# Performance work log

Hardware: AMD Instinct MI355X
Metric: run time of the kernel (lower is better)

## Reference

```python
import jax, jax.numpy as jnp
import numpy as np

N = 65536      # nodes
E = 1048576    # edges (avg degree 16)
L = 24         # input_length == lstm input size == lstm num_layers
H = 64         # lstm hidden


def _lin_init(key, fi, fo):
    return jax.random.normal(key, (fi, fo), jnp.float32) / np.sqrt(fi)


def setup_inputs() -> dict:
    key = jax.random.key(0)
    ks = iter(jax.random.split(key, 64))
    d = {}
    d["x"] = jax.random.normal(next(ks), (N, 421 + L), jnp.float32)
    d["edge_index"] = jax.random.randint(next(ks), (2, E), 0, N)

    def lin(fi, fo):
        return _lin_init(next(ks), fi, fo), jnp.zeros((fo,), jnp.float32)

    d["poi1_W"], d["poi1_b"] = lin(13, 64)
    d["poi2_W"], d["poi2_b"] = lin(64, 64)
    d["svi1_W"], d["svi1_b"] = lin(365, 128)
    d["svi2_W"], d["svi2_b"] = lin(128, 128)
    d["all1_W"], d["all1_b"] = lin(192, 128)
    d["all2_W"], d["all2_b"] = lin(128, 128)
    for name, fi, fo in (("gat1", 128, 128), ("gat2", 128, 128), ("gat3", 128, 64)):
        d[name + "_W"], d[name + "_b"] = lin(fi, fo)
        d[name + "_asrc"] = jax.random.normal(next(ks), (fo,), jnp.float32) / np.sqrt(fo)
        d[name + "_adst"] = jax.random.normal(next(ks), (fo,), jnp.float32) / np.sqrt(fo)
    d["lstm_Wih0"] = jax.random.normal(next(ks), (L, 4 * H), jnp.float32) / np.sqrt(L)
    d["lstm_Wih"] = jax.random.normal(next(ks), (L - 1, H, 4 * H), jnp.float32) / np.sqrt(H)
    d["lstm_Whh"] = jax.random.normal(next(ks), (L, H, 4 * H), jnp.float32) / np.sqrt(H)
    d["lstm_b"] = jnp.zeros((L, 4 * H), jnp.float32)
    d["time1_W"], d["time1_b"] = lin(64, 64)
    d["time2_W"], d["time2_b"] = lin(64, 64)
    d["lin1_W"], d["lin1_b"] = lin(128, 64)
    d["lin2_W"], d["lin2_b"] = lin(64, 64)
    d["lin3_W"], d["lin3_b"] = lin(64, 1)
    return d


def _gat(h_in, W, a_src, a_dst, b, src, dst, n):
    # PyG GATConv (1 head): gather -> per-edge attn -> segment softmax -> scatter
    h = h_in @ W                                   # [N, F]
    s = h @ a_src                                  # [N]
    t = h @ a_dst                                  # [N]
    e = jax.nn.leaky_relu(s[src] + t[dst], 0.2)    # [E']
    m = jax.ops.segment_max(e, dst, num_segments=n)
    ee = jnp.exp(e - m[dst])
    denom = jax.ops.segment_sum(ee, dst, num_segments=n)
    alpha = ee / denom[dst]
    out = jax.ops.segment_sum(h[src] * alpha[:, None], dst, num_segments=n)
    return out + b


def _forward(x, poi1_W, poi1_b, poi2_W, poi2_b, svi1_W, svi1_b, svi2_W, svi2_b,
             all1_W, all1_b, all2_W, all2_b,
             gat1_W, gat1_b, gat1_asrc, gat1_adst,
             gat2_W, gat2_b, gat2_asrc, gat2_adst,
             gat3_W, gat3_b, gat3_asrc, gat3_adst,
             lstm_Wih0, lstm_Wih, lstm_Whh, lstm_b,
             time1_W, time1_b, time2_W, time2_b,
             lin1_W, lin1_b, lin2_W, lin2_b, lin3_W, lin3_b,
             edge_index):
    n = x.shape[0]
    relu = jax.nn.relu
    # feature-branch MLPs
    x_poi = relu(relu(x[:, 3:16] @ poi1_W + poi1_b) @ poi2_W + poi2_b)
    x_svi = relu(relu(x[:, 56:421] @ svi1_W + svi1_b) @ svi2_W + svi2_b)
    h = jnp.concatenate([x_poi, x_svi], axis=1)
    h = relu(relu(h @ all1_W + all1_b) @ all2_W + all2_b)
    # add self loops once (PyG GATConv default add_self_loops=True)
    loops = jnp.arange(n, dtype=edge_index.dtype)
    src = jnp.concatenate([edge_index[0], loops])
    dst = jnp.concatenate([edge_index[1], loops])
    h = relu(_gat(h, gat1_W, gat1_asrc, gat1_adst, gat1_b, src, dst, n))
    h = relu(_gat(h, gat2_W, gat2_asrc, gat2_adst, gat2_b, src, dst, n))
    h = relu(_gat(h, gat3_W, gat3_asrc, gat3_adst, gat3_b, src, dst, n))
    # stacked LSTM over the single timestep t (h0=c0=0 -> f gate & Whh contribute 0)
    inp = x[:, 421:]                               # [N, L]
    hs = []
    for l in range(L):
        Wih = lstm_Wih0 if l == 0 else lstm_Wih[l - 1]
        gates = inp @ Wih + lstm_b[l]              # [N, 4H], torch gate order i,f,g,o
        i, f, g, o = jnp.split(gates, 4, axis=-1)
        c = jax.nn.sigmoid(i) * jnp.tanh(g)
        h_l = jax.nn.sigmoid(o) * jnp.tanh(c)
        hs.append(h_l)
        inp = h_l
    t = hs[2]                                      # hn[2]
    t = relu(relu(t @ time1_W + time1_b) @ time2_W + time2_b)
    z = jnp.concatenate([h, t], axis=1)            # [N, 128]
    z = relu(z @ lin1_W + lin1_b)
    z = relu(z @ lin2_W + lin2_b)
    return z @ lin3_W + lin3_b                     # [N, 1]


def reference(x, edge_index, poi1_W, poi1_b, poi2_W, poi2_b, svi1_W, svi1_b,
              svi2_W, svi2_b, all1_W, all1_b, all2_W, all2_b,
              gat1_W, gat1_b, gat1_asrc, gat1_adst,
              gat2_W, gat2_b, gat2_asrc, gat2_adst,
              gat3_W, gat3_b, gat3_asrc, gat3_adst,
              lstm_Wih0, lstm_Wih, lstm_Whh, lstm_b,
              time1_W, time1_b, time2_W, time2_b,
              lin1_W, lin1_b, lin2_W, lin2_b, lin3_W, lin3_b):
    return _forward(x, poi1_W, poi1_b, poi2_W, poi2_b, svi1_W, svi1_b, svi2_W, svi2_b,
                    all1_W, all1_b, all2_W, all2_b,
                    gat1_W, gat1_b, gat1_asrc, gat1_adst,
                    gat2_W, gat2_b, gat2_asrc, gat2_adst,
                    gat3_W, gat3_b, gat3_asrc, gat3_adst,
                    lstm_Wih0, lstm_Wih, lstm_Whh, lstm_b,
                    time1_W, time1_b, time2_W, time2_b,
                    lin1_W, lin1_b, lin2_W, lin2_b, lin3_W, lin3_b,
                    edge_index)
```

## Files before the change

### kernel.cpp

```cpp
#include <hip/hip_runtime.h>
#include <math.h>

#define DEV __device__ __forceinline__

typedef __attribute__((ext_vector_type(8))) short short8;
typedef __attribute__((ext_vector_type(4))) float f32x4;
typedef float f32x4u __attribute__((ext_vector_type(4), aligned(4)));
typedef __attribute__((ext_vector_type(4))) unsigned int u32x4;
typedef __attribute__((ext_vector_type(4))) _Float16 h16x4;

#define NEG_BIG (-3.0e38f)
#define CAPB 4096
#define CHUNK 4096

DEV float sigm(float x) { return 1.0f / (1.0f + __expf(-x)); }
DEV float leaky(float e) { return (e >= 0.0f) ? e : 0.2f * e; }

DEV void split_bf16(const float f[8], short8& hi, short8& lo) {
#pragma unroll
  for (int i = 0; i < 8; ++i) {
    unsigned u = __builtin_bit_cast(unsigned, f[i]);
    hi[i] = (short)(u >> 16);
    float h = __builtin_bit_cast(float, u & 0xffff0000u);
    float r = f[i] - h;
    lo[i] = (short)(__builtin_bit_cast(unsigned, r) >> 16);
  }
}

DEV unsigned packsplit(float v) {
  unsigned u = __builtin_bit_cast(unsigned, v);
  unsigned hf = u & 0xffff0000u;
  float r = v - __builtin_bit_cast(float, hf);
  return hf | (__builtin_bit_cast(unsigned, r) >> 16);
}

DEV void unpack_pk(const u32x4 p0, const u32x4 p1, short8& hi, short8& lo) {
  u32x4 h, l;
  h[0] = __builtin_amdgcn_perm(p0[1], p0[0], 0x07060302u);
  h[1] = __builtin_amdgcn_perm(p0[3], p0[2], 0x07060302u);
  h[2] = __builtin_amdgcn_perm(p1[1], p1[0], 0x07060302u);
  h[3] = __builtin_amdgcn_perm(p1[3], p1[2], 0x07060302u);
  l[0] = __builtin_amdgcn_perm(p0[1], p0[0], 0x05040100u);
  l[1] = __builtin_amdgcn_perm(p0[3], p0[2], 0x05040100u);
  l[2] = __builtin_amdgcn_perm(p1[1], p1[0], 0x05040100u);
  l[3] = __builtin_amdgcn_perm(p1[3], p1[2], 0x05040100u);
  hi = __builtin_bit_cast(short8, h);
  lo = __builtin_bit_cast(short8, l);
}

template <int G, int MT, int NT>
DEV void mfma_grp(f32x4 (&acc)[MT][NT], const short8 (&ah)[MT],
                  const short8 (&al)[MT], const short8 (&bh)[4],
                  const short8 (&bl)[4]) {
#pragma unroll
  for (int mt = 0; mt < MT; ++mt)
#pragma unroll
    for (int j = 0; j < 4; ++j) {
      acc[mt][G * 4 + j] = __builtin_amdgcn_mfma_f32_16x16x32_bf16(
          ah[mt], bh[j], acc[mt][G * 4 + j], 0, 0, 0);
      acc[mt][G * 4 + j] = __builtin_amdgcn_mfma_f32_16x16x32_bf16(
          ah[mt], bl[j], acc[mt][G * 4 + j], 0, 0, 0);
      acc[mt][G * 4 + j] = __builtin_amdgcn_mfma_f32_16x16x32_bf16(
          al[mt], bh[j], acc[mt][G * 4 + j], 0, 0, 0);
    }
}


__global__ void fill_i32_kernel(int* p, int v, int n) {
  int i = blockIdx.x * blockDim.x + threadIdx.x;
  if (i < n) p[i] = v;
}


__global__ __launch_bounds__(256) void bucket_bin(
    const int* __restrict__ ei, int* __restrict__ bucket_cnt,
    unsigned* __restrict__ ebuf, int E, int Et) {
  __shared__ unsigned stage[CHUNK];
  __shared__ int hist[512], rbase[512], lcur[512];
  const int tid = threadIdx.x;
  const long long e0 = (long long)blockIdx.x * CHUNK;
  const int nalive = (int)((Et - e0) < CHUNK ? (Et - e0) : CHUNK);
  for (int i = tid; i < 512; i += 256) hist[i] = 0;
  __syncthreads();
  for (int k = tid; k < nalive; k += 256) {
    long long e = e0 + k;
    int s, d;
    if (e < E) { s = ei[e]; d = ei[E + e]; } else { s = (int)(e - E); d = s; }
    unsigned p = (unsigned)s | ((unsigned)d << 16);
    stage[k] = p;
    atomicAdd(&hist[d >> 7], 1);
  }
  __syncthreads();
  for (int i = tid; i < 512; i += 256) {
    int c = hist[i];
    rbase[i] = c ? atomicAdd(&bucket_cnt[i], c) : 0;
    lcur[i] = 0;
  }
  __syncthreads();
  for (int k = tid; k < nalive; k += 256) {
    unsigned p = stage[k];
    int b = (int)(p >> 23);
    int lofs = atomicAdd(&lcur[b], 1);
    int pos = rbase[b] + lofs;
    if (pos < CAPB) ebuf[(long long)b * CAPB + pos] = p;
  }
}

__global__ __launch_bounds__(512) void bucket_scan(
    const int* __restrict__ cnt, int* __restrict__ start, int Et) {
  __shared__ int sh[512];
  int tid = threadIdx.x;
  int v = cnt[tid];
  sh[tid] = v;
  __syncthreads();
  int val = v;
  for (int off = 1; off < 512; off <<= 1) {
    int add = (tid >= off) ? sh[tid - off] : 0;
    __syncthreads();
    val += add;
    sh[tid] = val;
    __syncthreads();
  }
  start[tid] = val - v;
  if (tid == 511) start[512] = Et;
}

__global__ __launch_bounds__(128) void bucket_csr(
    const unsigned* __restrict__ ebuf, const int* __restrict__ bucket_cnt,
    const int* __restrict__ bucket_start, int* __restrict__ row_start,
    int* __restrict__ srcs, int N, int Et) {
  __shared__ unsigned stage[CAPB];
  __shared__ int hist[128], hbase[128], lcur[128];
  const int b = blockIdx.x, tid = threadIdx.x;
  int cnt = bucket_cnt[b];
  cnt = cnt < CAPB ? cnt : CAPB;
  const int gbase = bucket_start[b];
  hist[tid] = 0;
  __syncthreads();
  const unsigned* eb = ebuf + (long long)b * CAPB;
  for (int k = tid; k < cnt; k += 128) {
    unsigned p = eb[k];
    stage[k] = p;
    atomicAdd(&hist[(p >> 16) & 127], 1);
  }
  __syncthreads();
  int v = hist[tid];
  hbase[tid] = v;
  __syncthreads();
  int val = v;
  for (int off = 1; off < 128; off <<= 1) {
    int add = (tid >= off) ? hbase[tid - off] : 0;
    __syncthreads();
    val += add;
    hbase[tid] = val;
    __syncthreads();
  }
  int ex = val - v;
  row_start[b * 128 + tid] = gbase + ex;
  __syncthreads();
  hbase[tid] = ex;
  lcur[tid] = 0;
  __syncthreads();
  for (int k = tid; k < cnt; k += 128) {
    unsigned p = stage[k];
    int o = (p >> 16) & 127;
    int lofs = atomicAdd(&lcur[o], 1);
    srcs[gbase + hbase[o] + lofs] = (int)(p & 0xffffu);
  }
  if (b == 0 && tid == 0) row_start[N] = Et;
}

struct WJobs {
  const float* W[16];
  short* hi[16];
  short* lo[16];
  int K[16];
  int M16[16];
  int ldw[16];
  int skip[16];
  int tile0[16];
};

__global__ __launch_bounds__(64) void wsplit_all(WJobs jb, int njobs) {
  int b = blockIdx.x;
  int ji = 0;
#pragma unroll
  for (int i = 1; i < 16; ++i)
    if (i < njobs && b >= jb.tile0[i]) ji = i;
  int t = b - jb.tile0[ji];
  int M16 = jb.M16[ji];
  int kc = t / M16, ntG = t % M16;
  int K = jb.K[ji], ldw = jb.ldw[ji];
  const float* __restrict__ W = jb.W[ji];

  int lane = threadIdx.x;
  int kb = kc * 32 + (lane >> 4) * 8;
  int c = ntG * 16 + (lane & 15);
  if (jb.skip[ji] && c >= 64) c += 64;
  float f[8];
#pragma unroll
  for (int j = 0; j < 8; ++j) {
    int k = kb + j;
    f[j] = (k < K) ? W[(long long)k * ldw + c] : 0.0f;
  }
  short8 h, l;
  split_bf16(f, h, l);
  long long off = ((long long)t * 64 + lane) * 8;
  *(short8*)(jb.hi[ji] + off) = h;
  *(short8*)(jb.lo[ji] + off) = l;
}


template <int MT, int NT, int APK>
DEV void gemm_loop(const void* __restrict__ Av, long long abase, int lda,
                   const short* __restrict__ wh, const short* __restrict__ wl,
                   int K, int KC, f32x4 (&acc)[MT][NT]) {
  const int lane = threadIdx.x;
  const int m = lane & 15, q = lane >> 4;
#pragma unroll
  for (int i = 0; i < MT; ++i)
#pragma unroll
    for (int j = 0; j < NT; ++j) acc[i][j] = (f32x4)(0.0f);

  u32x4 pA[MT][2];
  float fA[MT][8];

  auto loadA = [&](int kc) {
#pragma unroll
    for (int mt = 0; mt < MT; ++mt) {
      if (APK == 1) {
        const unsigned* ap =
            (const unsigned*)Av + (abase + mt * 16 + m) * lda + kc * 32 + q * 8;
        pA[mt][0] = *(const u32x4*)ap;
        pA[mt][1] = *(const u32x4*)(ap + 4);
      } else {
        const float* ap =
            (const float*)Av + (abase + mt * 16 + m) * lda + kc * 32 + q * 8;
        if (kc * 32 + 32 <= K) {
          f32x4u p0 = *(const f32x4u*)ap;
          f32x4u p1 = *(const f32x4u*)(ap + 4);
#pragma unroll
          for (int j = 0; j < 4; ++j) { fA[mt][j] = p0[j]; fA[mt][4 + j] = p1[j]; }
        } else {
#pragma unroll
          for (int j = 0; j < 8; ++j) {
            int k = kc * 32 + q * 8 + j;
            fA[mt][j] = (k < K) ? ap[j] : 0.0f;
          }
        }
      }
    }
  };

  short8 ah[MT], al[MT];
  auto unpackA = [&]() {
#pragma unroll
    for (int mt = 0; mt < MT; ++mt) {
      if (APK == 1)
        unpack_pk(pA[mt][0], pA[mt][1], ah[mt], al[mt]);
      else
        split_bf16(fA[mt], ah[mt], al[mt]);
    }
  };

  short8 bh0[4], bl0[4], bh1[4], bl1[4];
  auto loadB = [&](short8 (&bh)[4], short8 (&bl)[4], int kc, int gg) {
#pragma unroll
    for (int j = 0; j < 4; ++j) {
      long long off = (((long long)kc * NT + (gg * 4 + j)) * 64 + lane) * 8;
      bh[j] = *(const short8*)(wh + off);
      bl[j] = *(const short8*)(wl + off);
    }
  };

  if constexpr (NT == 4) {
    loadA(0);
    loadB(bh0, bl0, 0, 0);
    int kc = 0;
    for (; kc + 2 <= KC; kc += 2) {
      unpackA();
      loadB(bh1, bl1, kc + 1, 0);
      loadA(kc + 1);
      mfma_grp<0, MT, NT>(acc, ah, al, bh0, bl0);
      unpackA();
      if (kc + 2 < KC) {
        loadB(bh0, bl0, kc + 2, 0);
        loadA(kc + 2);
      }
      mfma_grp<0, MT, NT>(acc, ah, al, bh1, bl1);
    }
    if (kc < KC) {
      unpackA();
      mfma_grp<0, MT, NT>(acc, ah, al, bh0, bl0);
    }
  } else {
    loadA(0);
    loadB(bh0, bl0, 0, 0);
    for (int kc = 0; kc < KC; ++kc) {
      unpackA();
      loadB(bh1, bl1, kc, 1);
      if (kc + 1 < KC) loadA(kc + 1);
      mfma_grp<0, MT, NT>(acc, ah, al, bh0, bl0);
      if (kc + 1 < KC) loadB(bh0, bl0, kc + 1, 0);
      mfma_grp<1, MT, NT>(acc, ah, al, bh1, bl1);
    }
  }
}


template <int MT, int NT>
DEV void epi_packed(const f32x4 (&acc)[MT][NT], const float* bias,
                    unsigned* C, int ldc, long long r0, int act) {
  const int lane = threadIdx.x;
  const int m = lane & 15, q = lane >> 4;
#pragma unroll
  for (int nt = 0; nt < NT; ++nt) {
    int col = nt * 16 + m;
    float b = bias ? bias[col] : 0.0f;
#pragma unroll
    for (int mt = 0; mt < MT; ++mt) {
      long long rb = r0 + mt * 16 + q * 4;
#pragma unroll
      for (int reg = 0; reg < 4; ++reg) {
        float v = acc[mt][nt][reg] + b;
        if (act) v = fmaxf(v, 0.0f);
        C[(rb + reg) * ldc + col] = packsplit(v);
      }
    }
  }
}

template <int MT, int NT>
DEV void epi_lds(const f32x4 (&acc)[MT][NT], const float* bias,
                 unsigned* L, int S) {
  const int lane = threadIdx.x;
  const int m = lane & 15, q = lane >> 4;
#pragma unroll
  for (int nt = 0; nt < NT; ++nt) {
    int col = nt * 16 + m;
    float b = bias[col];
#pragma unroll
    for (int mt = 0; mt < MT; ++mt)
#pragma unroll
      for (int reg = 0; reg < 4; ++reg) {
        float v = fmaxf(acc[mt][nt][reg] + b, 0.0f);
        L[(mt * 16 + q * 4 + reg) * S + col] = packsplit(v);
      }
  }
}

struct GemmArgs {
  const void* A; const short* wh; const short* wl; const float* bias;
  void* C; const float* asrc; const float* adst; float* sOut; float* tOut;
  int lda, ldc, K, KC, act;
};

template <int MT, int NT, int APK, int OPK, int STE>
__global__ __launch_bounds__(64) void gemm_mfma(GemmArgs g) {
  const int lane = threadIdx.x;
  const int m = lane & 15, q = lane >> 4;
  const long long r0 = (long long)blockIdx.x * (MT * 16);
  f32x4 acc[MT][NT];
  gemm_loop<MT, NT, APK>(g.A, r0, g.lda, g.wh, g.wl, g.K, g.KC, acc);

#pragma unroll
  for (int nt = 0; nt < NT; ++nt) {
    int col = nt * 16 + m;
    float bsv = g.bias ? g.bias[col] : 0.0f;
#pragma unroll
    for (int mt = 0; mt < MT; ++mt) {
      long long rb = r0 + mt * 16 + q * 4;
#pragma unroll
      for (int reg = 0; reg < 4; ++reg) {
        float v = acc[mt][nt][reg] + bsv;
        if (g.act == 1) v = fmaxf(v, 0.0f);
        if (OPK == 1)
          ((unsigned*)g.C)[(rb + reg) * g.ldc + col] = packsplit(v);
        else if (OPK == 2)
          ((_Float16*)g.C)[(rb + reg) * g.ldc + col] = (_Float16)v;
        else
          ((float*)g.C)[(rb + reg) * g.ldc + col] = v;
      }
    }
  }

  if (STE == 1) {
    float as[NT], ad[NT];
#pragma unroll
    for (int nt = 0; nt < NT; ++nt) {
      int col = nt * 16 + m;
      as[nt] = g.asrc[col];
      ad[nt] = g.adst[col];
    }
#pragma unroll
    for (int mt = 0; mt < MT; ++mt)
#pragma unroll
      for (int reg = 0; reg < 4; ++reg) {
        float ps = 0.0f, pt = 0.0f;
#pragma unroll
        for (int nt = 0; nt < NT; ++nt) {
          ps = fmaf(acc[mt][nt][reg], as[nt], ps);
          pt = fmaf(acc[mt][nt][reg], ad[nt], pt);
        }
#pragma unroll
        for (int off = 1; off < 16; off <<= 1) {
          ps += __shfl_xor(ps, off, 64);
          pt += __shfl_xor(pt, off, 64);
        }
        if (m == 0) {
          long long r = r0 + mt * 16 + q * 4 + reg;
          g.sOut[r] = ps;
          g.tOut[r] = pt;
        }
      }
  }
}


struct PairJob {
  const void* A; int lda, K1;
  const short *w1h, *w1l; const float* b1;
  const short *w2h, *w2l; const float* b2; int K2;
  unsigned* C; int ldc;
};

template <int NT1, int APK1, int NT2>
DEV void pair_body(const PairJob& j, int bid, unsigned* lbuf) {
  constexpr int S = NT1 * 16 + 4;
  const long long r0 = (long long)bid * 32;
  {
    f32x4 acc[2][NT1];
    gemm_loop<2, NT1, APK1>(j.A, r0, j.lda, j.w1h, j.w1l, j.K1,
                            (j.K1 + 31) / 32, acc);
    epi_lds<2, NT1>(acc, j.b1, lbuf, S);
  }
  {
    f32x4 acc[2][NT2];
    gemm_loop<2, NT2, 1>(lbuf, 0, S, j.w2h, j.w2l, j.K2, (j.K2 + 31) / 32, acc);
    epi_packed<2, NT2>(acc, j.b2, j.C, j.ldc, r0, 1);
  }
}

template <int NT1, int APK1, int NT2>
__global__ __launch_bounds__(64) void pair_kernel(PairJob j) {
  __shared__ __align__(16) unsigned lbuf[32 * 132];
  pair_body<NT1, APK1, NT2>(j, blockIdx.x, lbuf);
}


struct ChainJob {
  const float* x; int lda;
  const short *w0h, *w0l; const float* b0;
  const short *w1h, *w1l; const float* b1;
  const short *w2h, *w2l; const float* b2;
  const short *t1h, *t1l; const float* tb1;
  const short *t2h, *t2l; const float* tb2;
  unsigned* C; int ldc;
};

template <int APK>
DEV void lstm_loop(const void* __restrict__ Av, long long abase, int lda,
                   const short* __restrict__ wh, const short* __restrict__ wl,
                   int K, int KC, f32x4 (&acc)[12]) {
  const int lane = threadIdx.x;
  const int m = lane & 15, q = lane >> 4;
#pragma unroll
  for (int j = 0; j < 12; ++j) acc[j] = (f32x4)(0.0f);

  u32x4 pA[2];
  float fA[8];

  auto loadA = [&](int kc) {
    if (APK == 1) {
      const unsigned* ap =
          (const unsigned*)Av + (abase + m) * lda + kc * 32 + q * 8;
      pA[0] = *(const u32x4*)ap;
      pA[1] = *(const u32x4*)(ap + 4);
    } else {
      const float* ap = (const float*)Av + (abase + m) * lda + kc * 32 + q * 8;
      if (kc * 32 + 32 <= K) {
        f32x4u p0 = *(const f32x4u*)ap;
        f32x4u p1 = *(const f32x4u*)(ap + 4);
#pragma unroll
        for (int j = 0; j < 4; ++j) { fA[j] = p0[j]; fA[4 + j] = p1[j]; }
      } else {
#pragma unroll
        for (int j = 0; j < 8; ++j) {
          int k = kc * 32 + q * 8 + j;
          fA[j] = (k < K) ? ap[j] : 0.0f;
        }
      }
    }
  };

  short8 bh0, bl0, bh1, bl1;
  auto loadB = [&](short8& bh, short8& bl, int kc, int nt) {
    long long off = (((long long)kc * 12 + nt) * 64 + lane) * 8;
    bh = *(const short8*)(wh + off);
    bl = *(const short8*)(wl + off);
  };

  loadA(0);
  loadB(bh0, bl0, 0, 0);
  for (int kc = 0; kc < KC; ++kc) {
    short8 ah, al;
    if (APK == 1)
      unpack_pk(pA[0], pA[1], ah, al);
    else
      split_bf16(fA, ah, al);
    loadB(bh1, bl1, kc, 1);
    if (kc + 1 < KC) loadA(kc + 1);
    const int kn = (kc + 1 < KC) ? kc + 1 : kc;
#pragma unroll
    for (int nt = 0; nt < 12; ++nt) {
      short8& cbh = (nt & 1) ? bh1 : bh0;
      short8& cbl = (nt & 1) ? bl1 : bl0;
      acc[nt] = __builtin_amdgcn_mfma_f32_16x16x32_bf16(ah, cbh, acc[nt], 0, 0, 0);
      acc[nt] = __builtin_amdgcn_mfma_f32_16x16x32_bf16(ah, cbl, acc[nt], 0, 0, 0);
      acc[nt] = __builtin_amdgcn_mfma_f32_16x16x32_bf16(al, cbh, acc[nt], 0, 0, 0);
      if (nt + 2 < 12)
        loadB((nt & 1) ? bh1 : bh0, (nt & 1) ? bl1 : bl0, kc, nt + 2);
      else if (nt + 2 == 12)
        loadB(bh0, bl0, kn, 0);
    }
  }
}

DEV void lstm_epi_lds(const f32x4 (&acc)[12], const float* bias,
                      unsigned* L, int S) {
  const int lane = threadIdx.x;
  const int m = lane & 15, q = lane >> 4;
#pragma unroll
  for (int nt = 0; nt < 4; ++nt) {
    int col = nt * 16 + m;
    float bi = bias[col], bg = bias[128 + col], bo = bias[192 + col];
#pragma unroll
    for (int reg = 0; reg < 4; ++reg) {
      float gi = acc[nt][reg] + bi;
      float gg = acc[nt + 4][reg] + bg;
      float go = acc[nt + 8][reg] + bo;
      float cc = sigm(gi) * tanhf(gg);
      L[(q * 4 + reg) * S + col] = packsplit(sigm(go) * tanhf(cc));
    }
  }
}

DEV void chain_body(const ChainJob& c, int bid, unsigned* lbuf) {
  constexpr int S = 68;
  const long long r0 = (long long)bid * 16;
  unsigned* H0 = lbuf;
  unsigned* H1 = lbuf + 16 * S;
  {
    f32x4 acc[12];
    lstm_loop<0>(c.x, r0, c.lda, c.w0h, c.w0l, 24, 1, acc);
    lstm_epi_lds(acc, c.b0, H0, S);
  }
  {
    f32x4 acc[12];
    lstm_loop<1>(H0, 0, S, c.w1h, c.w1l, 64, 2, acc);
    lstm_epi_lds(acc, c.b1, H1, S);
  }
  {
    f32x4 acc[12];
    lstm_loop<1>(H1, 0, S, c.w2h, c.w2l, 64, 2, acc);
    lstm_epi_lds(acc, c.b2, H0, S);
  }
  {
    f32x4 acc[1][4];
    gemm_loop<1, 4, 1>(H0, 0, S, c.t1h, c.t1l, 64, 2, acc);
    epi_lds<1, 4>(acc, c.tb1, H1, S);
  }
  {
    f32x4 acc[1][4];
    gemm_loop<1, 4, 1>(H1, 0, S, c.t2h, c.t2l, 64, 2, acc);
    epi_packed<1, 4>(acc, c.tb2, c.C, c.ldc, r0, 1);
  }
}


__global__ __launch_bounds__(64) void tower_combo(PairJob svi, PairJob poi,
                                                  ChainJob ch, int nA, int nAB) {
  __shared__ __align__(16) unsigned lbuf[32 * 132];
  int bid = blockIdx.x;
  if (bid < nA)
    pair_body<8, 0, 8>(svi, bid, lbuf);
  else if (bid < nAB)
    pair_body<4, 0, 4>(poi, bid - nA, lbuf);
  else
    chain_body(ch, bid - nAB, lbuf);
}


struct HeadJob {
  const void* A; int lda, K1;
  const short *w1h, *w1l; const float* b1;
  const short *w2h, *w2l; const float* b2; int K2;
  const float* w3; const float* b3; float* out;
};

__global__ __launch_bounds__(64) void head_kernel(HeadJob j) {
  __shared__ __align__(16) unsigned lbuf[32 * 68];
  constexpr int S = 68;
  const int lane = threadIdx.x;
  const int m = lane & 15, q = lane >> 4;
  const long long r0 = (long long)blockIdx.x * 32;
  {
    f32x4 acc[2][4];
    gemm_loop<2, 4, 1>(j.A, r0, j.lda, j.w1h, j.w1l, j.K1, (j.K1 + 31) / 32, acc);
    epi_lds<2, 4>(acc, j.b1, lbuf, S);
  }
  {
    f32x4 acc[2][4];
    gemm_loop<2, 4, 1>(lbuf, 0, S, j.w2h, j.w2l, j.K2, (j.K2 + 31) / 32, acc);
    float w3[4], bs[4];
#pragma unroll
    for (int nt = 0; nt < 4; ++nt) {
      int col = nt * 16 + m;
      w3[nt] = j.w3[col];
      bs[nt] = j.b2[col];
    }
#pragma unroll
    for (int mt = 0; mt < 2; ++mt)
#pragma unroll
      for (int reg = 0; reg < 4; ++reg) {
        float ps = 0.0f;
#pragma unroll
        for (int nt = 0; nt < 4; ++nt) {
          float v = fmaxf(acc[mt][nt][reg] + bs[nt], 0.0f);
          ps = fmaf(v, w3[nt], ps);
        }
#pragma unroll
        for (int off = 1; off < 16; off <<= 1) ps += __shfl_xor(ps, off, 64);
        if (m == 0) j.out[r0 + mt * 16 + q * 4 + reg] = ps + j.b3[0];
      }
  }
}


template <int FO, int OPK>
__global__ __launch_bounds__(256) void gat_agg(
    const _Float16* __restrict__ G, const float* __restrict__ s,
    const float* __restrict__ t, const int* __restrict__ row_start,
    const int* __restrict__ srcs, const float* __restrict__ bias,
    void* __restrict__ outv, int ldc) {
  constexpr int CAP = 128;
  constexpr int LPE = FO / 4;
  constexpr int EPW = 64 / LPE;
  __shared__ float ecache[4][CAP];
  __shared__ int icache[4][CAP];
  const int wv = threadIdx.x >> 6;
  const int lane = threadIdx.x & 63;
  const int d = blockIdx.x * 4 + wv;
  const int start = row_start[d], end = row_start[d + 1];
  const float td = t[d];

  float m = NEG_BIG, dsum = 0.0f;
  for (int j = start + lane; j < end; j += 64) {
    int sj = srcs[j];
    float e = leaky(s[sj] + td);
    int idx = j - start;
    if (idx < CAP) { ecache[wv][idx] = e; icache[wv][idx] = sj; }
    float mn = fmaxf(m, e);
    dsum = dsum * __expf(m - mn) + __expf(e - mn);
    m = mn;
  }
#pragma unroll
  for (int off = 32; off; off >>= 1) {
    float mo = __shfl_xor(m, off, 64);
    float dso = __shfl_xor(dsum, off, 64);
    float mn = fmaxf(m, mo);
    dsum = dsum * __expf(m - mn) + dso * __expf(mo - mn);
    m = mn;
  }
  const float inv = 1.0f / dsum;

  const int deg = end - start;
  const int capdeg = deg < CAP ? deg : CAP;
  for (int idx = lane; idx < capdeg; idx += 64)
    ecache[wv][idx] = __expf(ecache[wv][idx] - m) * inv;
  __syncthreads();

  const int grp = lane / LPE, cl = lane % LPE;
  const _Float16* __restrict__ Gc = G + cl * 4;
  float a0 = 0.0f, a1 = 0.0f, a2 = 0.0f, a3 = 0.0f;
  int idx = grp;
  for (; idx + 3 * EPW < capdeg; idx += 4 * EPW) {
    const int i1 = idx + EPW, i2 = idx + 2 * EPW, i3 = idx + 3 * EPW;
    int s0 = icache[wv][idx], s1 = icache[wv][i1];
    int s2 = icache[wv][i2], s3 = icache[wv][i3];
    float l0 = ecache[wv][idx], l1 = ecache[wv][i1];
    float l2 = ecache[wv][i2], l3 = ecache[wv][i3];
    h16x4 g0 = *(const h16x4*)(Gc + (long long)s0 * FO);
    h16x4 g1 = *(const h16x4*)(Gc + (long long)s1 * FO);
    h16x4 g2 = *(const h16x4*)(Gc + (long long)s2 * FO);
    h16x4 g3 = *(const h16x4*)(Gc + (long long)s3 * FO);
    a0 = fmaf(l0, (float)g0[0], a0); a1 = fmaf(l0, (float)g0[1], a1);
    a2 = fmaf(l0, (float)g0[2], a2); a3 = fmaf(l0, (float)g0[3], a3);
    a0 = fmaf(l1, (float)g1[0], a0); a1 = fmaf(l1, (float)g1[1], a1);
    a2 = fmaf(l1, (float)g1[2], a2); a3 = fmaf(l1, (float)g1[3], a3);
    a0 = fmaf(l2, (float)g2[0], a0); a1 = fmaf(l2, (float)g2[1], a1);
    a2 = fmaf(l2, (float)g2[2], a2); a3 = fmaf(l2, (float)g2[3], a3);
    a0 = fmaf(l3, (float)g3[0], a0); a1 = fmaf(l3, (float)g3[1], a1);
    a2 = fmaf(l3, (float)g3[2], a2); a3 = fmaf(l3, (float)g3[3], a3);
  }
  for (; idx + EPW < capdeg; idx += 2 * EPW) {
    const int i1 = idx + EPW;
    int s0 = icache[wv][idx], s1 = icache[wv][i1];
    float l0 = ecache[wv][idx], l1 = ecache[wv][i1];
    h16x4 g0 = *(const h16x4*)(Gc + (long long)s0 * FO);
    h16x4 g1 = *(const h16x4*)(Gc + (long long)s1 * FO);
    a0 = fmaf(l0, (float)g0[0], a0); a1 = fmaf(l0, (float)g0[1], a1);
    a2 = fmaf(l0, (float)g0[2], a2); a3 = fmaf(l0, (float)g0[3], a3);
    a0 = fmaf(l1, (float)g1[0], a0); a1 = fmaf(l1, (float)g1[1], a1);
    a2 = fmaf(l1, (float)g1[2], a2); a3 = fmaf(l1, (float)g1[3], a3);
  }
  for (; idx < capdeg; idx += EPW) {
    int s0 = icache[wv][idx];
    float l0 = ecache[wv][idx];
    h16x4 g0 = *(const h16x4*)(Gc + (long long)s0 * FO);
    a0 = fmaf(l0, (float)g0[0], a0); a1 = fmaf(l0, (float)g0[1], a1);
    a2 = fmaf(l0, (float)g0[2], a2); a3 = fmaf(l0, (float)g0[3], a3);
  }
  for (; idx < deg; idx += EPW) {
    int s0 = srcs[start + idx];
    float l0 = __expf(leaky(s[s0] + td) - m) * inv;
    h16x4 g0 = *(const h16x4*)(Gc + (long long)s0 * FO);
    a0 = fmaf(l0, (float)g0[0], a0); a1 = fmaf(l0, (float)g0[1], a1);
    a2 = fmaf(l0, (float)g0[2], a2); a3 = fmaf(l0, (float)g0[3], a3);
  }
#pragma unroll
  for (int off = 32; off >= LPE; off >>= 1) {
    a0 += __shfl_xor(a0, off, 64);
    a1 += __shfl_xor(a1, off, 64);
    a2 += __shfl_xor(a2, off, 64);
    a3 += __shfl_xor(a3, off, 64);
  }
  if (grp == 0) {
    f32x4u bs = *(const f32x4u*)(bias + cl * 4);
    float v0 = fmaxf(a0 + bs[0], 0.0f);
    float v1 = fmaxf(a1 + bs[1], 0.0f);
    float v2 = fmaxf(a2 + bs[2], 0.0f);
    float v3 = fmaxf(a3 + bs[3], 0.0f);
    if (OPK == 1) {
      u32x4 pv;
      pv[0] = packsplit(v0); pv[1] = packsplit(v1);
      pv[2] = packsplit(v2); pv[3] = packsplit(v3);
      *(u32x4*)((unsigned*)outv + (long long)d * ldc + cl * 4) = pv;
    } else {
      f32x4u v; v[0] = v0; v[1] = v1; v[2] = v2; v[3] = v3;
      *(f32x4u*)((float*)outv + (long long)d * ldc + cl * 4) = v;
    }
  }
}


struct WSplit { const short* hi; const short* lo; };

extern "C" void kernel_launch(void* const* d_in, const int* in_sizes, int n_in,
                              void* d_out, int out_size, void* d_ws, size_t ws_size,
                              hipStream_t stream) {
  const int N = 65536, E = 1048576;
  const int Et = E + N;

  const float* x        = (const float*)d_in[0];
  const int*   ei       = (const int*)d_in[1];
  const float* poi1_W   = (const float*)d_in[2];
  const float* poi1_b   = (const float*)d_in[3];
  const float* poi2_W   = (const float*)d_in[4];
  const float* poi2_b   = (const float*)d_in[5];
  const float* svi1_W   = (const float*)d_in[6];
  const float* svi1_b   = (const float*)d_in[7];
  const float* svi2_W   = (const float*)d_in[8];
  const float* svi2_b   = (const float*)d_in[9];
  const float* all1_W   = (const float*)d_in[10];
  const float* all1_b   = (const float*)d_in[11];
  const float* all2_W   = (const float*)d_in[12];
  const float* all2_b   = (const float*)d_in[13];
  const float* gat1_W   = (const float*)d_in[14];
  const float* gat1_b   = (const float*)d_in[15];
  const float* gat1_as  = (const float*)d_in[16];
  const float* gat1_ad  = (const float*)d_in[17];
  const float* gat2_W   = (const float*)d_in[18];
  const float* gat2_b   = (const float*)d_in[19];
  const float* gat2_as  = (const float*)d_in[20];
  const float* gat2_ad  = (const float*)d_in[21];
  const float* gat3_W   = (const float*)d_in[22];
  const float* gat3_b   = (const float*)d_in[23];
  const float* gat3_as  = (const float*)d_in[24];
  const float* gat3_ad  = (const float*)d_in[25];
  const float* lstm_Wih0= (const float*)d_in[26];
  const float* lstm_Wih = (const float*)d_in[27];
  const float* lstm_b   = (const float*)d_in[29];
  const float* time1_W  = (const float*)d_in[30];
  const float* time1_b  = (const float*)d_in[31];
  const float* time2_W  = (const float*)d_in[32];
  const float* time2_b  = (const float*)d_in[33];
  const float* lin1_W   = (const float*)d_in[34];
  const float* lin1_b   = (const float*)d_in[35];
  const float* lin2_W   = (const float*)d_in[36];
  const float* lin2_b   = (const float*)d_in[37];
  const float* lin3_W   = (const float*)d_in[38];
  const float* lin3_b   = (const float*)d_in[39];
  float* out = (float*)d_out;

  float* wsf   = (float*)d_ws;
  float* R192  = wsf;
  float* RA    = R192 + (size_t)N * 192;
  float* RB    = RA + (size_t)N * 128;
  float* Rz    = RB + (size_t)N * 128;
  float* sArr  = Rz + (size_t)N * 128;
  float* tArr  = sArr + N;
  int* ints         = (int*)(tArr + N);
  int* row_start    = ints;
  int* srcs         = row_start + (N + 1);
  int* bucket_cnt   = srcs + Et;
  int* bucket_start = bucket_cnt + 512;
  unsigned* ebuf    = (unsigned*)(bucket_start + 513);
  short* pool = (short*)(((uintptr_t)(ebuf + 512 * CAPB) + 15) & ~(uintptr_t)15);

  WJobs jb{};
  int nj = 0, tiles = 0;
  auto split = [&](const float* W, int K, int M, int ldw, int skip) -> WSplit {
    int KC = (K + 31) / 32;
    size_t sz = (size_t)KC * M * 32;
    short* hi = pool; pool += sz;
    short* lo = pool; pool += sz;
    jb.W[nj] = W; jb.hi[nj] = hi; jb.lo[nj] = lo;
    jb.K[nj] = K; jb.M16[nj] = M / 16; jb.ldw[nj] = ldw; jb.skip[nj] = skip;
    jb.tile0[nj] = tiles;
    tiles += KC * (M / 16);
    ++nj;
    return {hi, lo};
  };

  auto mkg = [&](const void* A, int lda, WSplit w, const float* bias, void* C,
                 int ldc, int K, int act, const float* as_ = nullptr,
                 const float* ad_ = nullptr, float* sO = nullptr,
                 float* tO = nullptr) -> GemmArgs {
    GemmArgs g;
    g.A = A; g.lda = lda; g.wh = w.hi; g.wl = w.lo; g.bias = bias;
    g.C = C; g.ldc = ldc; g.K = K; g.KC = (K + 31) / 32; g.act = act;
    g.asrc = as_; g.adst = ad_; g.sOut = sO; g.tOut = tO;
    return g;
  };

  WSplit wpoi1 = split(poi1_W, 13, 64, 64, 0);
  WSplit wpoi2 = split(poi2_W, 64, 64, 64, 0);
  WSplit wsvi1 = split(svi1_W, 365, 128, 128, 0);
  WSplit wsvi2 = split(svi2_W, 128, 128, 128, 0);
  WSplit wall1 = split(all1_W, 192, 128, 128, 0);
  WSplit wall2 = split(all2_W, 128, 128, 128, 0);
  WSplit wg1   = split(gat1_W, 128, 128, 128, 0);
  WSplit wg2   = split(gat2_W, 128, 128, 128, 0);
  WSplit wg3   = split(gat3_W, 128, 64, 64, 0);
  WSplit wls0  = split(lstm_Wih0, 24, 192, 256, 1);
  WSplit wls1  = split(lstm_Wih, 64, 192, 256, 1);
  WSplit wls2  = split(lstm_Wih + 64 * 256, 64, 192, 256, 1);
  WSplit wt1   = split(time1_W, 64, 64, 64, 0);
  WSplit wt2   = split(time2_W, 64, 64, 64, 0);
  WSplit wl1   = split(lin1_W, 128, 64, 64, 0);
  WSplit wl2   = split(lin2_W, 64, 64, 64, 0);
  hipLaunchKernelGGL(wsplit_all, dim3(tiles), dim3(64), 0, stream, jb, nj);

  const int TB = 256;
  const int GB = N / 32;
  const int CB = N / 16;

  hipLaunchKernelGGL(fill_i32_kernel, dim3(2), dim3(TB), 0, stream,
                     bucket_cnt, 0, 512);
  hipLaunchKernelGGL(bucket_bin, dim3((Et + CHUNK - 1) / CHUNK), dim3(256),
                     0, stream, ei, bucket_cnt, ebuf, E, Et);
  hipLaunchKernelGGL(bucket_scan, dim3(1), dim3(512), 0, stream,
                     bucket_cnt, bucket_start, Et);
  hipLaunchKernelGGL(bucket_csr, dim3(512), dim3(128), 0, stream,
                     ebuf, bucket_cnt, bucket_start, row_start, srcs, N, Et);

  _Float16* Gh = (_Float16*)RA;

  PairJob svi;
  svi.A = x + 56; svi.lda = 445; svi.K1 = 365;
  svi.w1h = wsvi1.hi; svi.w1l = wsvi1.lo; svi.b1 = svi1_b;
  svi.w2h = wsvi2.hi; svi.w2l = wsvi2.lo; svi.b2 = svi2_b; svi.K2 = 128;
  svi.C = (unsigned*)R192 + 64; svi.ldc = 192;
  PairJob poi;
  poi.A = x + 3; poi.lda = 445; poi.K1 = 13;
  poi.w1h = wpoi1.hi; poi.w1l = wpoi1.lo; poi.b1 = poi1_b;
  poi.w2h = wpoi2.hi; poi.w2l = wpoi2.lo; poi.b2 = poi2_b; poi.K2 = 64;
  poi.C = (unsigned*)R192; poi.ldc = 192;
  ChainJob ch;
  ch.x = x + 421; ch.lda = 445;
  ch.w0h = wls0.hi; ch.w0l = wls0.lo; ch.b0 = lstm_b;
  ch.w1h = wls1.hi; ch.w1l = wls1.lo; ch.b1 = lstm_b + 256;
  ch.w2h = wls2.hi; ch.w2l = wls2.lo; ch.b2 = lstm_b + 512;
  ch.t1h = wt1.hi; ch.t1l = wt1.lo; ch.tb1 = time1_b;
  ch.t2h = wt2.hi; ch.t2l = wt2.lo; ch.tb2 = time2_b;
  ch.C = (unsigned*)Rz + 64; ch.ldc = 128;
  hipLaunchKernelGGL(tower_combo, dim3(GB + GB + CB), dim3(64), 0, stream,
                     svi, poi, ch, GB, GB + GB);

  PairJob allp;
  allp.A = R192; allp.lda = 192; allp.K1 = 192;
  allp.w1h = wall1.hi; allp.w1l = wall1.lo; allp.b1 = all1_b;
  allp.w2h = wall2.hi; allp.w2l = wall2.lo; allp.b2 = all2_b; allp.K2 = 128;
  allp.C = (unsigned*)RB; allp.ldc = 128;
  hipLaunchKernelGGL((pair_kernel<8, 1, 8>), dim3(GB), dim3(64), 0, stream,
                     allp);

  const int aggBlocks = N / 4;

  hipLaunchKernelGGL((gemm_mfma<2, 8, 1, 2, 1>), dim3(GB), dim3(64), 0, stream,
                     mkg(RB, 128, wg1, nullptr, Gh, 128, 128, 0,
                         gat1_as, gat1_ad, sArr, tArr));
  hipLaunchKernelGGL((gat_agg<128, 1>), dim3(aggBlocks), dim3(256), 0, stream,
                     Gh, sArr, tArr, row_start, srcs, gat1_b, RB, 128);
  hipLaunchKernelGGL((gemm_mfma<2, 8, 1, 2, 1>), dim3(GB), dim3(64), 0, stream,
                     mkg(RB, 128, wg2, nullptr, Gh, 128, 128, 0,
                         gat2_as, gat2_ad, sArr, tArr));
  hipLaunchKernelGGL((gat_agg<128, 1>), dim3(aggBlocks), dim3(256), 0, stream,
                     Gh, sArr, tArr, row_start, srcs, gat2_b, RB, 128);
  hipLaunchKernelGGL((gemm_mfma<2, 4, 1, 2, 1>), dim3(GB), dim3(64), 0, stream,
                     mkg(RB, 128, wg3, nullptr, Gh, 64, 128, 0,
                         gat3_as, gat3_ad, sArr, tArr));
  hipLaunchKernelGGL((gat_agg<64, 1>), dim3(aggBlocks), dim3(256), 0, stream,
                     Gh, sArr, tArr, row_start, srcs, gat3_b, Rz, 128);

  HeadJob hd;
  hd.A = Rz; hd.lda = 128; hd.K1 = 128;
  hd.w1h = wl1.hi; hd.w1l = wl1.lo; hd.b1 = lin1_b;
  hd.w2h = wl2.hi; hd.w2l = wl2.lo; hd.b2 = lin2_b; hd.K2 = 64;
  hd.w3 = lin3_W; hd.b3 = lin3_b; hd.out = out;
  hipLaunchKernelGGL(head_kernel, dim3(GB), dim3(64), 0, stream, hd);
}
```

Before: 583.0 us.

## Fuse GAT aggregation with next layer's projection GEMM in one kernel

Adds an agg_gemm kernel in which four waves each aggregate four destination rows into an LDS tile. Wave 0 then runs the next GAT layer's MFMA projection on that tile and also computes the attention scalars s and t. This removes the round trip of writing aggregated features to global memory and reading them back in separate gemm launches, and cuts two launches. In exchange, three of the four waves sit idle during the GEMM phase, and ping-pong buffers (Gh2, sB, tB) are added so the fused kernel never overwrites the inputs it is still reading.

```diff
diff --git a/kernel.cpp b/kernel.cpp
--- a/kernel.cpp
+++ b/kernel.cpp
@@ -215,7 +215,7 @@
 DEV void gemm_loop(const void* __restrict__ Av, long long abase, int lda,
                    const short* __restrict__ wh, const short* __restrict__ wl,
                    int K, int KC, f32x4 (&acc)[MT][NT]) {
-  const int lane = threadIdx.x;
+  const int lane = threadIdx.x & 63;
   const int m = lane & 15, q = lane >> 4;
 #pragma unroll
   for (int i = 0; i < MT; ++i)
@@ -311,7 +311,7 @@
 template <int MT, int NT>
 DEV void epi_packed(const f32x4 (&acc)[MT][NT], const float* bias,
                     unsigned* C, int ldc, long long r0, int act) {
-  const int lane = threadIdx.x;
+  const int lane = threadIdx.x & 63;
   const int m = lane & 15, q = lane >> 4;
 #pragma unroll
   for (int nt = 0; nt < NT; ++nt) {
@@ -333,7 +333,7 @@
 template <int MT, int NT>
 DEV void epi_lds(const f32x4 (&acc)[MT][NT], const float* bias,
                  unsigned* L, int S) {
-  const int lane = threadIdx.x;
+  const int lane = threadIdx.x & 63;
   const int m = lane & 15, q = lane >> 4;
 #pragma unroll
   for (int nt = 0; nt < NT; ++nt) {
@@ -462,7 +462,7 @@
 DEV void lstm_loop(const void* __restrict__ Av, long long abase, int lda,
                    const short* __restrict__ wh, const short* __restrict__ wl,
                    int K, int KC, f32x4 (&acc)[12]) {
-  const int lane = threadIdx.x;
+  const int lane = threadIdx.x & 63;
   const int m = lane & 15, q = lane >> 4;
 #pragma unroll
   for (int j = 0; j < 12; ++j) acc[j] = (f32x4)(0.0f);
@@ -528,7 +528,7 @@
 
 DEV void lstm_epi_lds(const f32x4 (&acc)[12], const float* bias,
                       unsigned* L, int S) {
-  const int lane = threadIdx.x;
+  const int lane = threadIdx.x & 63;
   const int m = lane & 15, q = lane >> 4;
 #pragma unroll
   for (int nt = 0; nt < 4; ++nt) {
@@ -749,6 +749,161 @@
     } else {
       f32x4u v; v[0] = v0; v[1] = v1; v[2] = v2; v[3] = v3;
       *(f32x4u*)((float*)outv + (long long)d * ldc + cl * 4) = v;
+    }
+  }
+}
+
+
+template <int NT2>
+__global__ __launch_bounds__(256) void agg_gemm(
+    const _Float16* __restrict__ G, const float* __restrict__ s,
+    const float* __restrict__ t, const int* __restrict__ row_start,
+    const int* __restrict__ srcs, const float* __restrict__ bias,
+    const short* __restrict__ w2h, const short* __restrict__ w2l,
+    _Float16* __restrict__ G2, int ldG2,
+    const float* __restrict__ as2, const float* __restrict__ ad2,
+    float* __restrict__ sOut, float* __restrict__ tOut) {
+  constexpr int CAP = 128;
+  constexpr int FO = 128;
+  constexpr int S = 132;
+  __shared__ float ecache[4][CAP];
+  __shared__ int icache[4][CAP];
+  __shared__ __align__(16) unsigned htile[16 * S];
+  const int wv = threadIdx.x >> 6;
+  const int lane = threadIdx.x & 63;
+  const long long r0 = (long long)blockIdx.x * 16;
+
+  for (int k = 0; k < 4; ++k) {
+    const int d = (int)r0 + wv * 4 + k;
+    const int start = row_start[d], end = row_start[d + 1];
+    const float td = t[d];
+
+    float m = NEG_BIG, dsum = 0.0f;
+    for (int j = start + lane; j < end; j += 64) {
+      int sj = srcs[j];
+      float e = leaky(s[sj] + td);
+      int idx = j - start;
+      if (idx < CAP) { ecache[wv][idx] = e; icache[wv][idx] = sj; }
+      float mn = fmaxf(m, e);
+      dsum = dsum * __expf(m - mn) + __expf(e - mn);
+      m = mn;
+    }
+#pragma unroll
+    for (int off = 32; off; off >>= 1) {
+      float mo = __shfl_xor(m, off, 64);
+      float dso = __shfl_xor(dsum, off, 64);
+      float mn = fmaxf(m, mo);
+      dsum = dsum * __expf(m - mn) + dso * __expf(mo - mn);
+      m = mn;
+    }
+    const float inv = 1.0f / dsum;
+
+    const int deg = end - start;
+    const int capdeg = deg < CAP ? deg : CAP;
+    for (int idx = lane; idx < capdeg; idx += 64)
+      ecache[wv][idx] = __expf(ecache[wv][idx] - m) * inv;
+    __syncthreads();
+
+    const int grp = lane >> 5, cl = lane & 31;
+    const _Float16* __restrict__ Gc = G + cl * 4;
+    float a0 = 0.0f, a1 = 0.0f, a2 = 0.0f, a3 = 0.0f;
+    int idx = grp;
+    for (; idx + 6 < capdeg; idx += 8) {
+      const int i1 = idx + 2, i2 = idx + 4, i3 = idx + 6;
+      int s0 = icache[wv][idx], s1 = icache[wv][i1];
+      int s2 = icache[wv][i2], s3 = icache[wv][i3];
+      float l0 = ecache[wv][idx], l1 = ecache[wv][i1];
+      float l2 = ecache[wv][i2], l3 = ecache[wv][i3];
+      h16x4 g0 = *(const h16x4*)(Gc + (long long)s0 * FO);
+      h16x4 g1 = *(const h16x4*)(Gc + (long long)s1 * FO);
+      h16x4 g2 = *(const h16x4*)(Gc + (long long)s2 * FO);
+      h16x4 g3 = *(const h16x4*)(Gc + (long long)s3 * FO);
+      a0 = fmaf(l0, (float)g0[0], a0); a1 = fmaf(l0, (float)g0[1], a1);
+      a2 = fmaf(l0, (float)g0[2], a2); a3 = fmaf(l0, (float)g0[3], a3);
+      a0 = fmaf(l1, (float)g1[0], a0); a1 = fmaf(l1, (float)g1[1], a1);
+      a2 = fmaf(l1, (float)g1[2], a2); a3 = fmaf(l1, (float)g1[3], a3);
+      a0 = fmaf(l2, (float)g2[0], a0); a1 = fmaf(l2, (float)g2[1], a1);
+      a2 = fmaf(l2, (float)g2[2], a2); a3 = fmaf(l2, (float)g2[3], a3);
+      a0 = fmaf(l3, (float)g3[0], a0); a1 = fmaf(l3, (float)g3[1], a1);
+      a2 = fmaf(l3, (float)g3[2], a2); a3 = fmaf(l3, (float)g3[3], a3);
+    }
+    for (; idx + 2 < capdeg; idx += 4) {
+      const int i1 = idx + 2;
+      int s0 = icache[wv][idx], s1 = icache[wv][i1];
+      float l0 = ecache[wv][idx], l1 = ecache[wv][i1];
+      h16x4 g0 = *(const h16x4*)(Gc + (long long)s0 * FO);
+      h16x4 g1 = *(const h16x4*)(Gc + (long long)s1 * FO);
+      a0 = fmaf(l0, (float)g0[0], a0); a1 = fmaf(l0, (float)g0[1], a1);
+      a2 = fmaf(l0, (float)g0[2], a2); a3 = fmaf(l0, (float)g0[3], a3);
+      a0 = fmaf(l1, (float)g1[0], a0); a1 = fmaf(l1, (float)g1[1], a1);
+      a2 = fmaf(l1, (float)g1[2], a2); a3 = fmaf(l1, (float)g1[3], a3);
+    }
+    for (; idx < capdeg; idx += 2) {
+      int s0 = icache[wv][idx];
+      float l0 = ecache[wv][idx];
+      h16x4 g0 = *(const h16x4*)(Gc + (long long)s0 * FO);
+      a0 = fmaf(l0, (float)g0[0], a0); a1 = fmaf(l0, (float)g0[1], a1);
+      a2 = fmaf(l0, (float)g0[2], a2); a3 = fmaf(l0, (float)g0[3], a3);
+    }
+    for (; idx < deg; idx += 2) {
+      int s0 = srcs[start + idx];
+      float l0 = __expf(leaky(s[s0] + td) - m) * inv;
+      h16x4 g0 = *(const h16x4*)(Gc + (long long)s0 * FO);
+      a0 = fmaf(l0, (float)g0[0], a0); a1 = fmaf(l0, (float)g0[1], a1);
+      a2 = fmaf(l0, (float)g0[2], a2); a3 = fmaf(l0, (float)g0[3], a3);
+    }
+    a0 += __shfl_xor(a0, 32, 64);
+    a1 += __shfl_xor(a1, 32, 64);
+    a2 += __shfl_xor(a2, 32, 64);
+    a3 += __shfl_xor(a3, 32, 64);
+    if (grp == 0) {
+      f32x4u bs = *(const f32x4u*)(bias + cl * 4);
+      u32x4 pv;
+      pv[0] = packsplit(fmaxf(a0 + bs[0], 0.0f));
+      pv[1] = packsplit(fmaxf(a1 + bs[1], 0.0f));
+      pv[2] = packsplit(fmaxf(a2 + bs[2], 0.0f));
+      pv[3] = packsplit(fmaxf(a3 + bs[3], 0.0f));
+      *(u32x4*)&htile[(wv * 4 + k) * S + cl * 4] = pv;
+    }
+  }
+  __syncthreads();
+
+  if (threadIdx.x < 64) {
+    const int m = lane & 15, q = lane >> 4;
+    f32x4 acc[1][NT2];
+    gemm_loop<1, NT2, 1>(htile, 0, S, w2h, w2l, 128, 4, acc);
+#pragma unroll
+    for (int nt = 0; nt < NT2; ++nt) {
+      int col = nt * 16 + m;
+#pragma unroll
+      for (int reg = 0; reg < 4; ++reg)
+        G2[(r0 + q * 4 + reg) * ldG2 + col] = (_Float16)acc[0][nt][reg];
+    }
+    float as[NT2], ad[NT2];
+#pragma unroll
+    for (int nt = 0; nt < NT2; ++nt) {
+      int col = nt * 16 + m;
+      as[nt] = as2[col];
+      ad[nt] = ad2[col];
+    }
+#pragma unroll
+    for (int reg = 0; reg < 4; ++reg) {
+      float ps = 0.0f, pt = 0.0f;
+#pragma unroll
+      for (int nt = 0; nt < NT2; ++nt) {
+        ps = fmaf(acc[0][nt][reg], as[nt], ps);
+        pt = fmaf(acc[0][nt][reg], ad[nt], pt);
+      }
+#pragma unroll
+      for (int off = 1; off < 16; off <<= 1) {
+        ps += __shfl_xor(ps, off, 64);
+        pt += __shfl_xor(pt, off, 64);
+      }
+      if (m == 0) {
+        long long r = r0 + q * 4 + reg;
+        sOut[r] = ps;
+        tOut[r] = pt;
+      }
     }
   }
 }
@@ -810,7 +965,9 @@
   float* Rz    = RB + (size_t)N * 128;
   float* sArr  = Rz + (size_t)N * 128;
   float* tArr  = sArr + N;
-  int* ints         = (int*)(tArr + N);
+  float* sB    = tArr + N;
+  float* tB    = sB + N;
+  int* ints         = (int*)(tB + N);
   int* row_start    = ints;
   int* srcs         = row_start + (N + 1);
   int* bucket_cnt   = srcs + Et;
@@ -875,7 +1032,8 @@
   hipLaunchKernelGGL(bucket_csr, dim3(512), dim3(128), 0, stream,
                      ebuf, bucket_cnt, bucket_start, row_start, srcs, N, Et);
 
-  _Float16* Gh = (_Float16*)RA;
+  _Float16* Gh  = (_Float16*)RA;
+  _Float16* Gh2 = (_Float16*)RB;
 
   PairJob svi;
   svi.A = x + 56; svi.lda = 445; svi.K1 = 365;
@@ -906,22 +1064,19 @@
   hipLaunchKernelGGL((pair_kernel<8, 1, 8>), dim3(GB), dim3(64), 0, stream,
                      allp);
 
-  const int aggBlocks = N / 4;
-
   hipLaunchKernelGGL((gemm_mfma<2, 8, 1, 2, 1>), dim3(GB), dim3(64), 0, stream,
                      mkg(RB, 128, wg1, nullptr, Gh, 128, 128, 0,
                          gat1_as, gat1_ad, sArr, tArr));
-  hipLaunchKernelGGL((gat_agg<128, 1>), dim3(aggBlocks), dim3(256), 0, stream,
-                     Gh, sArr, tArr, row_start, srcs, gat1_b, RB, 128);
-  hipLaunchKernelGGL((gemm_mfma<2, 8, 1, 2, 1>), dim3(GB), dim3(64), 0, stream,
-                     mkg(RB, 128, wg2, nullptr, Gh, 128, 128, 0,
-                         gat2_as, gat2_ad, sArr, tArr));
-  hipLaunchKernelGGL((gat_agg<128, 1>), dim3(aggBlocks), dim3(256), 0, stream,
-                     Gh, sArr, tArr, row_start, srcs, gat2_b, RB, 128);
-  hipLaunchKernelGGL((gemm_mfma<2, 4, 1, 2, 1>), dim3(GB), dim3(64), 0, stream,
-                     mkg(RB, 128, wg3, nullptr, Gh, 64, 128, 0,
-                         gat3_as, gat3_ad, sArr, tArr));
-  hipLaunchKernelGGL((gat_agg<64, 1>), dim3(aggBlocks), dim3(256), 0, stream,
+
+  hipLaunchKernelGGL((agg_gemm<8>), dim3(N / 16), dim3(256), 0, stream,
+                     Gh, sArr, tArr, row_start, srcs, gat1_b,
+                     wg2.hi, wg2.lo, Gh2, 128, gat2_as, gat2_ad, sB, tB);
+
+  hipLaunchKernelGGL((agg_gemm<4>), dim3(N / 16), dim3(256), 0, stream,
+                     Gh2, sB, tB, row_start, srcs, gat2_b,
+                     wg3.hi, wg3.lo, Gh, 64, gat3_as, gat3_ad, sArr, tArr);
+
+  hipLaunchKernelGGL((gat_agg<64, 1>), dim3(N / 4), dim3(256), 0, stream,
                      Gh, sArr, tArr, row_start, srcs, gat3_b, Rz, 128);
 
   HeadJob hd;
```

Result: slower. 622.0 us (+6.7%).
